# Optimization experiments

Measured on AMD Instinct MI355X. Metric: run time of the kernel, lower is better.

Reference implementation:

```python
import jax, jax.numpy as jnp
import numpy as np

B, S, D, H, E, K = 4, 2048, 1024, 2048, 8, 2
TEMP = 5.0
EPS = 1e-9


def setup_inputs() -> dict:
    key = jax.random.key(0)
    k_x, k_wg, k_w1, k_w2 = jax.random.split(key, 4)
    scale = 0.02
    return {
        "x": jax.random.normal(k_x, (B, S, D), dtype=jnp.float32),
        "Wg": jax.random.normal(k_wg, (D, E), dtype=jnp.float32) * scale,
        "bg": jnp.zeros((E,), dtype=jnp.float32),
        "W1": jax.random.normal(k_w1, (E, D, H), dtype=jnp.float32) * scale,
        "b1": jnp.zeros((E, H), dtype=jnp.float32),
        "W2": jax.random.normal(k_w2, (E, H, D), dtype=jnp.float32) * scale,
        "b2": jnp.zeros((E, D), dtype=jnp.float32),
    }


def reference(x, Wg, bg, W1, b1, W2, b2):
    # Gating: softmax over experts with temperature
    logits = jnp.einsum('bsd,de->bse', x, Wg) + bg  # [B,S,E]
    probs = jax.nn.softmax(logits / TEMP, axis=-1)
    # Top-k mask, renormalized (zeros for non-selected experts)
    vals, idx = jax.lax.top_k(probs, K)              # [B,S,K]
    onehot = jax.nn.one_hot(idx, E, dtype=x.dtype)   # [B,S,K,E]
    mask = jnp.einsum('bske,bsk->bse', onehot, vals) # scatter topk values
    gates = mask / (jnp.sum(mask, axis=-1, keepdims=True) + EPS)
    # Expert FFNs (dense over experts; gate weight is exactly 0 for unrouted)
    h = jax.nn.gelu(jnp.einsum('bsd,edh->besh', x, W1) + b1[None, :, None, :],
                    approximate=False)               # [B,E,S,H]
    out = jnp.einsum('besh,ehd->besd', h, W2) + b2[None, :, None, :]
    y = jnp.einsum('bse,besd->bsd', gates, out)      # weighted combine
    return y
```

## Files before the change

kernel.cpp:

```cpp
#include <hip/hip_runtime.h>
#include <stdint.h>

#define NTOK 8192
#define DIM  1024
#define HID  2048
#define NE   8
#define CAP  17408
#define TM 128
#define TN 128
#define TKK 64

typedef __bf16  bf16x8  __attribute__((ext_vector_type(8)));
typedef float   floatx4 __attribute__((ext_vector_type(4)));

__device__ __forceinline__ unsigned short f2bf(float f) {
  union { float f; unsigned u; } v; v.f = f;
  unsigned r = v.u + 0x7FFFu + ((v.u >> 16) & 1u);
  return (unsigned short)(r >> 16);
}

__device__ __forceinline__ void async_ld16(const unsigned short* g, unsigned short* l) {
  __builtin_amdgcn_global_load_lds(
      (const __attribute__((address_space(1))) unsigned int*)(const void*)g,
      (__attribute__((address_space(3))) unsigned int*)(void*)l, 16, 0, 0);
}

__global__ void transpose_cast_kernel(const float* __restrict__ src,
                                      unsigned short* __restrict__ dst,
                                      int R, int C) {
  __shared__ unsigned short T[64][65];
  int e = blockIdx.z;
  const float* S = src + (size_t)e * R * C;
  unsigned short* D2 = dst + (size_t)e * R * C;
  int c0 = blockIdx.x * 64;
  int r0 = blockIdx.y * 64;
  int col = threadIdx.x & 63;
  int rr  = threadIdx.x >> 6;
#pragma unroll
  for (int i = 0; i < 16; i++) {
    int r = rr + i * 4;
    T[col][r] = f2bf(S[(size_t)(r0 + r) * C + c0 + col]);
  }
  __syncthreads();
#pragma unroll
  for (int i = 0; i < 16; i++) {
    int r = rr + i * 4;
    D2[(size_t)(c0 + r) * R + r0 + col] = T[r][col];
  }
}

__global__ __launch_bounds__(256)
void gating_kernel(const float* __restrict__ x, const float* __restrict__ Wg,
                   const float* __restrict__ bg, int* __restrict__ tok_e,
                   float* __restrict__ tok_g, unsigned short* __restrict__ xb) {
  __shared__ float WgS[NE * DIM];
  int tid = threadIdx.x;
#pragma unroll
  for (int j = 0; j < NE * DIM / 256; j++) {
    int i = j * 256 + tid;
    WgS[(i & 7) * DIM + (i >> 3)] = Wg[i];
  }
  __syncthreads();
  int wave = tid >> 6;
  int lane = tid & 63;
#pragma unroll
  for (int ti = 0; ti < 2; ti++) {
    int t = blockIdx.x * 8 + wave * 2 + ti;
    const float* xr = x + (size_t)t * DIM;
    float p[NE];
#pragma unroll
    for (int e = 0; e < NE; e++) p[e] = 0.f;
#pragma unroll
    for (int it = 0; it < DIM / 256; it++) {
      int d = (it * 64 + lane) * 4;
      float4 xv = *(const float4*)&xr[d];
      uint2 o;
      o.x = (unsigned)f2bf(xv.x) | ((unsigned)f2bf(xv.y) << 16);
      o.y = (unsigned)f2bf(xv.z) | ((unsigned)f2bf(xv.w) << 16);
      *(uint2*)&xb[(size_t)t * DIM + d] = o;
#pragma unroll
      for (int e = 0; e < NE; e++) {
        float4 wv = *(const float4*)&WgS[e * DIM + d];
        p[e] += xv.x * wv.x + xv.y * wv.y + xv.z * wv.z + xv.w * wv.w;
      }
    }
#pragma unroll
    for (int e = 0; e < NE; e++) {
#pragma unroll
      for (int off = 32; off > 0; off >>= 1) p[e] += __shfl_xor(p[e], off);
    }
    if (lane == 0) {
      float s[NE];
      float m = -1e30f;
#pragma unroll
      for (int e = 0; e < NE; e++) { s[e] = (p[e] + bg[e]) * 0.2f; m = fmaxf(m, s[e]); }
      float sum = 0.f;
#pragma unroll
      for (int e = 0; e < NE; e++) { s[e] = expf(s[e] - m); sum += s[e]; }
      float inv = 1.0f / sum;
      int i0 = 0; float v0 = -1.f;
#pragma unroll
      for (int e = 0; e < NE; e++) { float pe = s[e] * inv; if (pe > v0) { v0 = pe; i0 = e; } }
      int i1 = -1; float v1 = -1.f;
#pragma unroll
      for (int e = 0; e < NE; e++) {
        if (e == i0) continue;
        float pe = s[e] * inv; if (pe > v1) { v1 = pe; i1 = e; }
      }
      float den = v0 + v1 + 1e-9f;
      tok_e[t * 2]     = i0; tok_g[t * 2]     = v0 / den;
      tok_e[t * 2 + 1] = i1; tok_g[t * 2 + 1] = v1 / den;
    }
  }
}

__global__ __launch_bounds__(256)
void count_kernel(const int* __restrict__ tok_e, int* __restrict__ cnt) {
  __shared__ int hist[NE];
  int tid = threadIdx.x;
  if (tid < NE) hist[tid] = 0;
  __syncthreads();
  int i0 = blockIdx.x * 512 + tid;
  atomicAdd(&hist[tok_e[i0]], 1);
  atomicAdd(&hist[tok_e[i0 + 256]], 1);
  __syncthreads();
  if (tid < NE) atomicAdd(&cnt[tid], hist[tid]);
}

__global__ void offsets_kernel(const int* __restrict__ cnt, int* __restrict__ seg) {
  if (threadIdx.x == 0 && blockIdx.x == 0) {
    int s = 0;
    for (int e = 0; e < NE; e++) { seg[e] = s; s += ((cnt[e] + TM - 1) / TM) * TM; }
    seg[NE] = s;
  }
}

__global__ __launch_bounds__(256)
void route_kernel(const int* __restrict__ tok_e, const float* __restrict__ tok_g,
                  const int* __restrict__ seg, int* __restrict__ cnt2,
                  int* __restrict__ token_row, float* __restrict__ gate_row,
                  int* __restrict__ tok_pos) {
  __shared__ int hist[NE];
  __shared__ int base[NE];
  int tid = threadIdx.x;
  if (tid < NE) hist[tid] = 0;
  __syncthreads();
  int t = blockIdx.x * 256 + tid;
  int e0 = tok_e[t * 2];
  int e1 = tok_e[t * 2 + 1];
  int r0 = atomicAdd(&hist[e0], 1);
  int r1 = atomicAdd(&hist[e1], 1);
  __syncthreads();
  if (tid < NE) base[tid] = atomicAdd(&cnt2[tid], hist[tid]);
  __syncthreads();
  int p0 = seg[e0] + base[e0] + r0;
  int p1 = seg[e1] + base[e1] + r1;
  token_row[p0] = t; gate_row[p0] = tok_g[t * 2];     tok_pos[t * 2]     = p0;
  token_row[p1] = t; gate_row[p1] = tok_g[t * 2 + 1]; tok_pos[t * 2 + 1] = p1;
}

__global__ __launch_bounds__(256)
void gemm1_kernel(const unsigned short* __restrict__ xb, const unsigned short* __restrict__ w1t,
                  const float* __restrict__ b1, const int* __restrict__ token_row,
                  const int* __restrict__ seg, const unsigned short* __restrict__ zbuf,
                  unsigned short* __restrict__ hbuf) {
  __shared__ __align__(16) unsigned short As[TM * TKK];
  __shared__ __align__(16) unsigned short Bs[TN * TKK];
  int row0 = blockIdx.y * TM;
  int total = seg[NE];
  if (row0 >= total) return;
  int e = 0;
  while (row0 >= seg[e + 1]) e++;
  int n0 = blockIdx.x * TN;
  int tid = threadIdx.x;
  int lane = tid & 63;
  int w = tid >> 6;
  int wm = tid >> 7;
  int wn = (tid >> 6) & 1;
  int lrow = lane >> 3;
  int lk   = (lane & 7) * 8;

  floatx4 zero4 = {0.f, 0.f, 0.f, 0.f};
  floatx4 acc[4][4];
#pragma unroll
  for (int a = 0; a < 4; a++)
#pragma unroll
    for (int b = 0; b < 4; b++) acc[a][b] = zero4;

  const unsigned short* w1e = w1t + (size_t)e * DIM * HID;
  const unsigned short* srcA[4];
  const unsigned short* srcB[4];
#pragma unroll
  for (int i = 0; i < 4; i++) {
    int r = w * 32 + i * 8 + lrow;
    int t = token_row[row0 + r];
    srcA[i] = (t >= 0 ? xb + (size_t)t * DIM : zbuf) + lk;
    srcB[i] = w1e + (size_t)(n0 + r) * DIM + lk;
  }

  int mr = lane & 15;
  int kq = (lane >> 4) * 8;

  for (int k0 = 0; k0 < DIM; k0 += TKK) {
#pragma unroll
    for (int i = 0; i < 4; i++) {
      async_ld16(srcA[i] + k0, &As[(w * 32 + i * 8 + lrow) * TKK + lk]);
      async_ld16(srcB[i] + k0, &Bs[(w * 32 + i * 8 + lrow) * TKK + lk]);
    }
    __syncthreads();
#pragma unroll
    for (int kk = 0; kk < TKK; kk += 32) {
      bf16x8 af[4], bfr[4];
#pragma unroll
      for (int im = 0; im < 4; im++)
        af[im] = *(const bf16x8*)&As[(wm * 64 + im * 16 + mr) * TKK + kk + kq];
#pragma unroll
      for (int in = 0; in < 4; in++)
        bfr[in] = *(const bf16x8*)&Bs[(wn * 64 + in * 16 + mr) * TKK + kk + kq];
#pragma unroll
      for (int im = 0; im < 4; im++)
#pragma unroll
        for (int in = 0; in < 4; in++)
          acc[im][in] = __builtin_amdgcn_mfma_f32_16x16x32_bf16(af[im], bfr[in], acc[im][in], 0, 0, 0);
    }
    __syncthreads();
  }
  int quad = lane >> 4;
  int c16 = lane & 15;
  const float* b1e = b1 + e * HID;
#pragma unroll
  for (int im = 0; im < 4; im++) {
    int rb = row0 + wm * 64 + im * 16 + quad * 4;
#pragma unroll
    for (int in = 0; in < 4; in++) {
      int c = n0 + wn * 64 + in * 16 + c16;
      float bias = b1e[c];
#pragma unroll
      for (int i = 0; i < 4; i++) {
        float v = acc[im][in][i] + bias;
        v = 0.5f * v * (1.0f + erff(v * 0.70710678118654752f));
        hbuf[(size_t)(rb + i) * HID + c] = f2bf(v);
      }
    }
  }
}

__global__ __launch_bounds__(256)
void gemm2_kernel(const unsigned short* __restrict__ hbuf, const unsigned short* __restrict__ w2t,
                  const float* __restrict__ b2, const float* __restrict__ gate_row,
                  const int* __restrict__ seg, unsigned short* __restrict__ obuf) {
  __shared__ __align__(16) unsigned short As[TM * TKK];
  __shared__ __align__(16) unsigned short Bs[TN * TKK];
  int row0 = blockIdx.y * TM;
  int total = seg[NE];
  if (row0 >= total) return;
  int e = 0;
  while (row0 >= seg[e + 1]) e++;
  int n0 = blockIdx.x * TN;
  int tid = threadIdx.x;
  int lane = tid & 63;
  int w = tid >> 6;
  int wm = tid >> 7;
  int wn = (tid >> 6) & 1;
  int lrow = lane >> 3;
  int lk   = (lane & 7) * 8;

  floatx4 zero4 = {0.f, 0.f, 0.f, 0.f};
  floatx4 acc[4][4];
#pragma unroll
  for (int a = 0; a < 4; a++)
#pragma unroll
    for (int b = 0; b < 4; b++) acc[a][b] = zero4;

  const unsigned short* w2e = w2t + (size_t)e * DIM * HID;
  const unsigned short* srcA[4];
  const unsigned short* srcB[4];
#pragma unroll
  for (int i = 0; i < 4; i++) {
    int r = w * 32 + i * 8 + lrow;
    srcA[i] = hbuf + (size_t)(row0 + r) * HID + lk;
    srcB[i] = w2e + (size_t)(n0 + r) * HID + lk;
  }

  int mr = lane & 15;
  int kq = (lane >> 4) * 8;

  for (int k0 = 0; k0 < HID; k0 += TKK) {
#pragma unroll
    for (int i = 0; i < 4; i++) {
      async_ld16(srcA[i] + k0, &As[(w * 32 + i * 8 + lrow) * TKK + lk]);
      async_ld16(srcB[i] + k0, &Bs[(w * 32 + i * 8 + lrow) * TKK + lk]);
    }
    __syncthreads();
#pragma unroll
    for (int kk = 0; kk < TKK; kk += 32) {
      bf16x8 af[4], bfr[4];
#pragma unroll
      for (int im = 0; im < 4; im++)
        af[im] = *(const bf16x8*)&As[(wm * 64 + im * 16 + mr) * TKK + kk + kq];
#pragma unroll
      for (int in = 0; in < 4; in++)
        bfr[in] = *(const bf16x8*)&Bs[(wn * 64 + in * 16 + mr) * TKK + kk + kq];
#pragma unroll
      for (int im = 0; im < 4; im++)
#pragma unroll
        for (int in = 0; in < 4; in++)
          acc[im][in] = __builtin_amdgcn_mfma_f32_16x16x32_bf16(af[im], bfr[in], acc[im][in], 0, 0, 0);
    }
    __syncthreads();
  }
  int quad = lane >> 4;
  int c16 = lane & 15;
  const float* b2e = b2 + e * DIM;
#pragma unroll
  for (int im = 0; im < 4; im++) {
    int rb = row0 + wm * 64 + im * 16 + quad * 4;
    float gs[4];
#pragma unroll
    for (int i = 0; i < 4; i++) gs[i] = gate_row[rb + i];
#pragma unroll
    for (int in = 0; in < 4; in++) {
      int c = n0 + wn * 64 + in * 16 + c16;
      float bias = b2e[c];
#pragma unroll
      for (int i = 0; i < 4; i++) {
        float val = gs[i] * (acc[im][in][i] + bias);
        obuf[(size_t)(rb + i) * DIM + c] = f2bf(val);
      }
    }
  }
}

__global__ void combine_kernel(const unsigned short* __restrict__ obuf,
                               const int* __restrict__ tok_pos,
                               float* __restrict__ y) {
  int idx = blockIdx.x * 256 + threadIdx.x;
  int t = idx >> 7;
  int c = (idx & 127) << 3;
  int p0 = tok_pos[t * 2];
  int p1 = tok_pos[t * 2 + 1];
  uint4 a = *(const uint4*)(obuf + (size_t)p0 * DIM + c);
  uint4 b = *(const uint4*)(obuf + (size_t)p1 * DIM + c);
  float out[8];
  unsigned au[4] = {a.x, a.y, a.z, a.w};
  unsigned bu[4] = {b.x, b.y, b.z, b.w};
#pragma unroll
  for (int i = 0; i < 4; i++) {
    union { unsigned u; float f; } lo0, hi0, lo1, hi1;
    lo0.u = au[i] << 16; hi0.u = au[i] & 0xFFFF0000u;
    lo1.u = bu[i] << 16; hi1.u = bu[i] & 0xFFFF0000u;
    out[i * 2]     = lo0.f + lo1.f;
    out[i * 2 + 1] = hi0.f + hi1.f;
  }
  float* yp = y + (size_t)t * DIM + c;
  *(float4*)yp       = *(float4*)&out[0];
  *(float4*)(yp + 4) = *(float4*)&out[4];
}

extern "C" void kernel_launch(void* const* d_in, const int* in_sizes, int n_in,
                              void* d_out, int out_size, void* d_ws, size_t ws_size,
                              hipStream_t stream) {
  const float* x  = (const float*)d_in[0];
  const float* Wg = (const float*)d_in[1];
  const float* bg = (const float*)d_in[2];
  const float* W1 = (const float*)d_in[3];
  const float* b1 = (const float*)d_in[4];
  const float* W2 = (const float*)d_in[5];
  const float* b2 = (const float*)d_in[6];
  float* y = (float*)d_out;
  char* ws = (char*)d_ws;

  constexpr size_t OFF_META = 0;
  constexpr size_t OFF_TOKE = 256;
  constexpr size_t OFF_TOKG = OFF_TOKE + (size_t)NTOK * 2 * 4;
  constexpr size_t OFF_TPOS = OFF_TOKG + (size_t)NTOK * 2 * 4;
  constexpr size_t OFF_TROW = OFF_TPOS + (size_t)NTOK * 2 * 4;
  constexpr size_t OFF_GROW = OFF_TROW + (size_t)CAP * 4;
  constexpr size_t OFF_ZB   = OFF_GROW + (size_t)CAP * 4;
  constexpr size_t OFF_XB   = OFF_ZB  + (size_t)DIM * 2;
  constexpr size_t OFF_W1T  = OFF_XB  + (size_t)NTOK * DIM * 2;
  constexpr size_t OFF_W2T  = OFF_W1T + (size_t)NE * DIM * HID * 2;
  constexpr size_t OFF_H    = OFF_W2T + (size_t)NE * DIM * HID * 2;
  constexpr size_t OFF_OBUF = OFF_XB;

  int* cnt        = (int*)(ws + OFF_META);
  int* cnt2       = (int*)(ws + OFF_META + 64);
  int* seg        = (int*)(ws + OFF_META + 128);
  int* tok_e      = (int*)(ws + OFF_TOKE);
  float* tok_g    = (float*)(ws + OFF_TOKG);
  int* tok_pos    = (int*)(ws + OFF_TPOS);
  int* token_row  = (int*)(ws + OFF_TROW);
  float* gate_row = (float*)(ws + OFF_GROW);
  unsigned short* zbuf = (unsigned short*)(ws + OFF_ZB);
  unsigned short* xb   = (unsigned short*)(ws + OFF_XB);
  unsigned short* w1t  = (unsigned short*)(ws + OFF_W1T);
  unsigned short* w2t  = (unsigned short*)(ws + OFF_W2T);
  unsigned short* hbuf = (unsigned short*)(ws + OFF_H);
  unsigned short* obuf = (unsigned short*)(ws + OFF_OBUF);

  hipMemsetAsync(ws, 0, 192, stream);
  hipMemsetAsync(token_row, 0xFF, (size_t)CAP * 4, stream);
  hipMemsetAsync(zbuf, 0, (size_t)DIM * 2, stream);

  transpose_cast_kernel<<<dim3(HID / 64, DIM / 64, NE), 256, 0, stream>>>(W1, w1t, DIM, HID);
  transpose_cast_kernel<<<dim3(DIM / 64, HID / 64, NE), 256, 0, stream>>>(W2, w2t, HID, DIM);
  gating_kernel<<<NTOK / 8, 256, 0, stream>>>(x, Wg, bg, tok_e, tok_g, xb);
  count_kernel<<<NTOK * 2 / 512, 256, 0, stream>>>(tok_e, cnt);
  offsets_kernel<<<1, 64, 0, stream>>>(cnt, seg);
  route_kernel<<<NTOK / 256, 256, 0, stream>>>(tok_e, tok_g, seg, cnt2, token_row, gate_row, tok_pos);
  gemm1_kernel<<<dim3(HID / TN, CAP / TM), 256, 0, stream>>>(xb, w1t, b1, token_row, seg, zbuf, hbuf);
  gemm2_kernel<<<dim3(DIM / TN, CAP / TM), 256, 0, stream>>>(hbuf, w2t, b2, gate_row, seg, obuf);
  combine_kernel<<<NTOK * DIM / 8 / 256, 256, 0, stream>>>(obuf, tok_pos, y);
}
```

Before: 499.9 us.

## Widen GEMM N-tile to 256, swap MFMA operands for vector stores, fast tanh GELU

Both expert GEMMs now use a 128x256 output tile per block, so each wave holds a 4x8 grid of 16x16 accumulators and each A tile is reused across twice as many columns. The MFMA operands are swapped so each lane ends up with four consecutive columns, which lets the epilogue load bias as a float4 and write four packed bf16 values in one store. The exact erf GELU is replaced by a tanh approximation built on exp2 and rcp, and launch bounds ask for two blocks per CU. The larger tile doubles the B shared-memory buffer and the accumulator register count, which may lower occupancy, and the GELU approximation changes numerics slightly.

New measurement: 477.4 us. -4.5%, faster.

```diff
diff --git a/kernel.cpp b/kernel.cpp
--- a/kernel.cpp
+++ b/kernel.cpp
@@ -7,7 +7,7 @@
 #define NE   8
 #define CAP  17408
 #define TM 128
-#define TN 128
+#define TN 256
 #define TKK 64
 
 typedef __bf16  bf16x8  __attribute__((ext_vector_type(8)));
@@ -23,6 +23,19 @@
   __builtin_amdgcn_global_load_lds(
       (const __attribute__((address_space(1))) unsigned int*)(const void*)g,
       (__attribute__((address_space(3))) unsigned int*)(void*)l, 16, 0, 0);
+}
+
+__device__ __forceinline__ float gelu_fast(float v) {
+  float g = 0.79788456080286536f * (v + 0.044715f * v * v * v);
+  float t = __builtin_amdgcn_exp2f(-2.8853900817779268f * g);
+  return v * __builtin_amdgcn_rcpf(1.0f + t);
+}
+
+__device__ __forceinline__ uint2 pack4bf(float a, float b, float c, float d) {
+  uint2 o;
+  o.x = (unsigned)f2bf(a) | ((unsigned)f2bf(b) << 16);
+  o.y = (unsigned)f2bf(c) | ((unsigned)f2bf(d) << 16);
+  return o;
 }
 
 __global__ void transpose_cast_kernel(const float* __restrict__ src,
@@ -74,10 +87,7 @@
     for (int it = 0; it < DIM / 256; it++) {
       int d = (it * 64 + lane) * 4;
       float4 xv = *(const float4*)&xr[d];
-      uint2 o;
-      o.x = (unsigned)f2bf(xv.x) | ((unsigned)f2bf(xv.y) << 16);
-      o.y = (unsigned)f2bf(xv.z) | ((unsigned)f2bf(xv.w) << 16);
-      *(uint2*)&xb[(size_t)t * DIM + d] = o;
+      *(uint2*)&xb[(size_t)t * DIM + d] = pack4bf(xv.x, xv.y, xv.z, xv.w);
 #pragma unroll
       for (int e = 0; e < NE; e++) {
         float4 wv = *(const float4*)&WgS[e * DIM + d];
@@ -159,7 +169,7 @@
   token_row[p1] = t; gate_row[p1] = tok_g[t * 2 + 1]; tok_pos[t * 2 + 1] = p1;
 }
 
-__global__ __launch_bounds__(256)
+__global__ __launch_bounds__(256, 2)
 void gemm1_kernel(const unsigned short* __restrict__ xb, const unsigned short* __restrict__ w1t,
                   const float* __restrict__ b1, const int* __restrict__ token_row,
                   const int* __restrict__ seg, const unsigned short* __restrict__ zbuf,
@@ -181,20 +191,24 @@
   int lk   = (lane & 7) * 8;
 
   floatx4 zero4 = {0.f, 0.f, 0.f, 0.f};
-  floatx4 acc[4][4];
+  floatx4 acc[4][8];
 #pragma unroll
   for (int a = 0; a < 4; a++)
 #pragma unroll
-    for (int b = 0; b < 4; b++) acc[a][b] = zero4;
+    for (int b = 0; b < 8; b++) acc[a][b] = zero4;
 
   const unsigned short* w1e = w1t + (size_t)e * DIM * HID;
   const unsigned short* srcA[4];
-  const unsigned short* srcB[4];
+  const unsigned short* srcB[8];
 #pragma unroll
   for (int i = 0; i < 4; i++) {
     int r = w * 32 + i * 8 + lrow;
     int t = token_row[row0 + r];
     srcA[i] = (t >= 0 ? xb + (size_t)t * DIM : zbuf) + lk;
+  }
+#pragma unroll
+  for (int i = 0; i < 8; i++) {
+    int r = w * 64 + i * 8 + lrow;
     srcB[i] = w1e + (size_t)(n0 + r) * DIM + lk;
   }
 
@@ -203,25 +217,26 @@
 
   for (int k0 = 0; k0 < DIM; k0 += TKK) {
 #pragma unroll
-    for (int i = 0; i < 4; i++) {
+    for (int i = 0; i < 4; i++)
       async_ld16(srcA[i] + k0, &As[(w * 32 + i * 8 + lrow) * TKK + lk]);
-      async_ld16(srcB[i] + k0, &Bs[(w * 32 + i * 8 + lrow) * TKK + lk]);
-    }
+#pragma unroll
+    for (int i = 0; i < 8; i++)
+      async_ld16(srcB[i] + k0, &Bs[(w * 64 + i * 8 + lrow) * TKK + lk]);
     __syncthreads();
 #pragma unroll
     for (int kk = 0; kk < TKK; kk += 32) {
-      bf16x8 af[4], bfr[4];
+      bf16x8 af[4], bfr[8];
 #pragma unroll
       for (int im = 0; im < 4; im++)
         af[im] = *(const bf16x8*)&As[(wm * 64 + im * 16 + mr) * TKK + kk + kq];
 #pragma unroll
-      for (int in = 0; in < 4; in++)
-        bfr[in] = *(const bf16x8*)&Bs[(wn * 64 + in * 16 + mr) * TKK + kk + kq];
+      for (int in = 0; in < 8; in++)
+        bfr[in] = *(const bf16x8*)&Bs[(wn * 128 + in * 16 + mr) * TKK + kk + kq];
 #pragma unroll
       for (int im = 0; im < 4; im++)
 #pragma unroll
-        for (int in = 0; in < 4; in++)
-          acc[im][in] = __builtin_amdgcn_mfma_f32_16x16x32_bf16(af[im], bfr[in], acc[im][in], 0, 0, 0);
+        for (int in = 0; in < 8; in++)
+          acc[im][in] = __builtin_amdgcn_mfma_f32_16x16x32_bf16(bfr[in], af[im], acc[im][in], 0, 0, 0);
     }
     __syncthreads();
   }
@@ -230,22 +245,21 @@
   const float* b1e = b1 + e * HID;
 #pragma unroll
   for (int im = 0; im < 4; im++) {
-    int rb = row0 + wm * 64 + im * 16 + quad * 4;
-#pragma unroll
-    for (int in = 0; in < 4; in++) {
-      int c = n0 + wn * 64 + in * 16 + c16;
-      float bias = b1e[c];
-#pragma unroll
-      for (int i = 0; i < 4; i++) {
-        float v = acc[im][in][i] + bias;
-        v = 0.5f * v * (1.0f + erff(v * 0.70710678118654752f));
-        hbuf[(size_t)(rb + i) * HID + c] = f2bf(v);
-      }
-    }
-  }
-}
-
-__global__ __launch_bounds__(256)
+    int r = row0 + wm * 64 + im * 16 + c16;
+#pragma unroll
+    for (int in = 0; in < 8; in++) {
+      int c = n0 + wn * 128 + in * 16 + quad * 4;
+      float4 bias = *(const float4*)&b1e[c];
+      float v0 = gelu_fast(acc[im][in][0] + bias.x);
+      float v1 = gelu_fast(acc[im][in][1] + bias.y);
+      float v2 = gelu_fast(acc[im][in][2] + bias.z);
+      float v3 = gelu_fast(acc[im][in][3] + bias.w);
+      *(uint2*)&hbuf[(size_t)r * HID + c] = pack4bf(v0, v1, v2, v3);
+    }
+  }
+}
+
+__global__ __launch_bounds__(256, 2)
 void gemm2_kernel(const unsigned short* __restrict__ hbuf, const unsigned short* __restrict__ w2t,
                   const float* __restrict__ b2, const float* __restrict__ gate_row,
                   const int* __restrict__ seg, unsigned short* __restrict__ obuf) {
@@ -266,19 +280,23 @@
   int lk   = (lane & 7) * 8;
 
   floatx4 zero4 = {0.f, 0.f, 0.f, 0.f};
-  floatx4 acc[4][4];
+  floatx4 acc[4][8];
 #pragma unroll
   for (int a = 0; a < 4; a++)
 #pragma unroll
-    for (int b = 0; b < 4; b++) acc[a][b] = zero4;
+    for (int b = 0; b < 8; b++) acc[a][b] = zero4;
 
   const unsigned short* w2e = w2t + (size_t)e * DIM * HID;
   const unsigned short* srcA[4];
-  const unsigned short* srcB[4];
+  const unsigned short* srcB[8];
 #pragma unroll
   for (int i = 0; i < 4; i++) {
     int r = w * 32 + i * 8 + lrow;
     srcA[i] = hbuf + (size_t)(row0 + r) * HID + lk;
+  }
+#pragma unroll
+  for (int i = 0; i < 8; i++) {
+    int r = w * 64 + i * 8 + lrow;
     srcB[i] = w2e + (size_t)(n0 + r) * HID + lk;
   }
 
@@ -287,25 +305,26 @@
 
   for (int k0 = 0; k0 < HID; k0 += TKK) {
 #pragma unroll
-    for (int i = 0; i < 4; i++) {
+    for (int i = 0; i < 4; i++)
       async_ld16(srcA[i] + k0, &As[(w * 32 + i * 8 + lrow) * TKK + lk]);
-      async_ld16(srcB[i] + k0, &Bs[(w * 32 + i * 8 + lrow) * TKK + lk]);
-    }
+#pragma unroll
+    for (int i = 0; i < 8; i++)
+      async_ld16(srcB[i] + k0, &Bs[(w * 64 + i * 8 + lrow) * TKK + lk]);
     __syncthreads();
 #pragma unroll
     for (int kk = 0; kk < TKK; kk += 32) {
-      bf16x8 af[4], bfr[4];
+      bf16x8 af[4], bfr[8];
 #pragma unroll
       for (int im = 0; im < 4; im++)
         af[im] = *(const bf16x8*)&As[(wm * 64 + im * 16 + mr) * TKK + kk + kq];
 #pragma unroll
-      for (int in = 0; in < 4; in++)
-        bfr[in] = *(const bf16x8*)&Bs[(wn * 64 + in * 16 + mr) * TKK + kk + kq];
+      for (int in = 0; in < 8; in++)
+        bfr[in] = *(const bf16x8*)&Bs[(wn * 128 + in * 16 + mr) * TKK + kk + kq];
 #pragma unroll
       for (int im = 0; im < 4; im++)
 #pragma unroll
-        for (int in = 0; in < 4; in++)
-          acc[im][in] = __builtin_amdgcn_mfma_f32_16x16x32_bf16(af[im], bfr[in], acc[im][in], 0, 0, 0);
+        for (int in = 0; in < 8; in++)
+          acc[im][in] = __builtin_amdgcn_mfma_f32_16x16x32_bf16(bfr[in], af[im], acc[im][in], 0, 0, 0);
     }
     __syncthreads();
   }
@@ -314,19 +333,17 @@
   const float* b2e = b2 + e * DIM;
 #pragma unroll
   for (int im = 0; im < 4; im++) {
-    int rb = row0 + wm * 64 + im * 16 + quad * 4;
-    float gs[4];
-#pragma unroll
-    for (int i = 0; i < 4; i++) gs[i] = gate_row[rb + i];
-#pragma unroll
-    for (int in = 0; in < 4; in++) {
-      int c = n0 + wn * 64 + in * 16 + c16;
-      float bias = b2e[c];
-#pragma unroll
-      for (int i = 0; i < 4; i++) {
-        float val = gs[i] * (acc[im][in][i] + bias);
-        obuf[(size_t)(rb + i) * DIM + c] = f2bf(val);
-      }
+    int r = row0 + wm * 64 + im * 16 + c16;
+    float gs = gate_row[r];
+#pragma unroll
+    for (int in = 0; in < 8; in++) {
+      int c = n0 + wn * 128 + in * 16 + quad * 4;
+      float4 bias = *(const float4*)&b2e[c];
+      float v0 = gs * (acc[im][in][0] + bias.x);
+      float v1 = gs * (acc[im][in][1] + bias.y);
+      float v2 = gs * (acc[im][in][2] + bias.z);
+      float v3 = gs * (acc[im][in][3] + bias.w);
+      *(uint2*)&obuf[(size_t)r * DIM + c] = pack4bf(v0, v1, v2, v3);
     }
   }
 }
```
